# Optimization experiments

Hardware: AMD Instinct MI355X
Metric: run time of the kernel (lower is better)

## Reference

```python
import jax, jax.numpy as jnp
import numpy as np
from jax import lax

SPATIAL = 4
PAD = 1
STRIDE = 1


def _route(x, rconv_w, rconv_b, fc_w, fc_b, num_experts):
    # x: (b, c, h, w); adaptive avg pool to (SPATIAL, SPATIAL) -- h,w divisible by SPATIAL
    b, c, h, w = x.shape
    pooled = x.reshape(b, c, SPATIAL, h // SPATIAL, SPATIAL, w // SPATIAL).mean(axis=(3, 5))
    # 1x1 conv: (b,c,s,s) x (rc,c) -> (b,rc,s,s)
    y = jnp.einsum('bcij,rc->brij', pooled, rconv_w) + rconv_b[None, :, None, None]
    y = jax.nn.relu(y).reshape(b, -1)                      # (b, rc*s*s)
    y = jax.nn.relu(y @ fc_w.T + fc_b)                     # (b, num_experts*c)
    y = y.reshape(b, num_experts, c)
    return jax.nn.sigmoid(y)                               # (b, k, c)


def _conv_per_sample(xi, wi):
    # xi: (c_in, h, w), wi: (c_out, c_in, kh, kw)
    out = lax.conv_general_dilated(
        xi[None], wi, window_strides=(STRIDE, STRIDE),
        padding=[(PAD, PAD), (PAD, PAD)],
        dimension_numbers=('NCHW', 'OIHW', 'NCHW'))
    return out[0]


def setup_inputs() -> dict:
    key = jax.random.key(0)
    ks = jax.random.split(key, 6)
    b, c_in, c_out, kk, ne = 16, 256, 256, 3, 3
    rc = max(c_in // 16, 16)  # reduction_channels = 16
    x = jax.random.normal(ks[0], (b, c_in, 64, 64), dtype=jnp.float32)
    expert_weight = jax.random.normal(ks[1], (ne, c_out, c_in, kk, kk), dtype=jnp.float32) * 0.02
    rconv_w = jax.random.normal(ks[2], (rc, c_in), dtype=jnp.float32) * 0.05
    rconv_b = jax.random.normal(ks[3], (rc,), dtype=jnp.float32) * 0.05
    fc_w = jax.random.normal(ks[4], (ne * c_in, rc * SPATIAL * SPATIAL), dtype=jnp.float32) * 0.05
    fc_b = jax.random.normal(ks[5], (ne * c_in,), dtype=jnp.float32) * 0.05
    return {"x": x, "expert_weight": expert_weight, "rconv_w": rconv_w,
            "rconv_b": rconv_b, "fc_w": fc_w, "fc_b": fc_b}


def reference(x, expert_weight, rconv_w, rconv_b, fc_w, fc_b):
    ne = expert_weight.shape[0]
    r = _route(x, rconv_w, rconv_b, fc_w, fc_b, ne)        # (b, k, c_in)
    # per-sample combined weights: routing scales input channels of each expert kernel
    w = jnp.einsum('bkc,kocij->bocij', r, expert_weight)    # (b, c_out, c_in, kh, kw)
    out = jax.vmap(_conv_per_sample)(x, w)                  # (b, c_out, h', w')
    return out
```

## Files before the change

kernel.cpp:

```cpp
#include <hip/hip_runtime.h>

#define B_   16
#define C_   256
#define OC_  256
#define H_   64
#define W_   64

typedef __attribute__((ext_vector_type(8))) __bf16 bf16x8;
typedef __attribute__((ext_vector_type(4))) float  f32x4;

__device__ __forceinline__ short f2bf(float f) {
    unsigned u = __float_as_uint(f);
    u += 0x7fffu + ((u >> 16) & 1u);
    return (short)(u >> 16);
}
__device__ __forceinline__ unsigned pk2(float a, float b) {
    return (unsigned(f2bf(a)) & 0xffffu) | (unsigned(f2bf(b)) << 16);
}
__device__ __forceinline__ void gll16(const void* g, void* l) {
    __builtin_amdgcn_global_load_lds(
        (const __attribute__((address_space(1))) unsigned int*)g,
        (__attribute__((address_space(3))) unsigned int*)l,
        16, 0, 0);
}

__global__ __launch_bounds__(256) void k_transpose_pool(
        const float* __restrict__ x, short* __restrict__ xt, float* __restrict__ pooled) {
    int y = blockIdx.x, b = blockIdx.y, t = threadIdx.x;
    int si = y >> 4;
    int lane = t & 63, wv = t >> 6;
    int xq = lane & 15, cw = lane >> 4;
    __shared__ float tile[64 * 67];

    for (int cc = 0; cc < 4; ++cc) {
        int cbase = cc * 64;
        if (cc) __syncthreads();
        #pragma unroll
        for (int r = 0; r < 4; ++r) {
            int c_l = r * 16 + wv * 4 + cw;
            float4 v = *(const float4*)&x[(((size_t)b * C_ + cbase + c_l) * H_ + y) * W_ + xq * 4];
            float* tp = &tile[c_l * 67 + xq * 4];
            tp[0] = v.x; tp[1] = v.y; tp[2] = v.z; tp[3] = v.w;
            float s = v.x + v.y + v.z + v.w;
            s += __shfl_xor(s, 1);
            s += __shfl_xor(s, 2);
            if ((lane & 3) == 0)
                atomicAdd(&pooled[((b * 4 + si) * 4 + (xq >> 2)) * 256 + cbase + c_l], s);
        }
        __syncthreads();
        #pragma unroll
        for (int r2 = 0; r2 < 2; ++r2) {
            int u = r2 * 256 + t;
            int xx = u >> 3, cgl = u & 7;
            float f[8];
            #pragma unroll
            for (int j = 0; j < 8; ++j) f[j] = tile[(cgl * 8 + j) * 67 + xx];
            uint4 pkv;
            pkv.x = pk2(f[0], f[1]); pkv.y = pk2(f[2], f[3]);
            pkv.z = pk2(f[4], f[5]); pkv.w = pk2(f[6], f[7]);
            *(uint4*)&xt[(((size_t)b * H_ + y) * W_ + xx) * C_ + cbase + cgl * 8] = pkv;
        }
    }
}

__global__ __launch_bounds__(256) void k_route(
        const float* __restrict__ pooled, const float* __restrict__ rconv_w,
        const float* __restrict__ rconv_b, const float* __restrict__ fc_w,
        const float* __restrict__ fc_b, float* __restrict__ r_buf) {
    int b = blockIdx.x;
    int t = threadIdx.x;
    __shared__ float pl[16][257];
    __shared__ float y1[256];

    #pragma unroll
    for (int q = 0; q < 16; ++q)
        pl[q][t] = pooled[b * 4096 + q * 256 + t] * (1.0f / 256.0f);
    __syncthreads();
    {
        int rcc = t >> 4, ss = t & 15;
        float acc = rconv_b[rcc];
        #pragma unroll 8
        for (int c = 0; c < 256; ++c)
            acc += pl[ss][c] * rconv_w[rcc * 256 + c];
        y1[rcc * 16 + ss] = fmaxf(acc, 0.f);
    }
    __syncthreads();
    for (int e0 = 0; e0 < 768; e0 += 256) {
        int e = e0 + t;
        float acc = fc_b[e];
        #pragma unroll 8
        for (int q = 0; q < 256; ++q)
            acc += y1[q] * fc_w[(size_t)e * 256 + q];
        acc = fmaxf(acc, 0.f);
        r_buf[(size_t)b * 768 + e] = 1.f / (1.f + __expf(-acc));
    }
}

__global__ __launch_bounds__(256) void k_combine(
        const float* __restrict__ E, const float* __restrict__ r_buf,
        short* __restrict__ wcomb) {
    int o = blockIdx.x;
    int b0 = blockIdx.y * 4;
    int t = threadIdx.x;
    __shared__ float eT[3][2304];
    #pragma unroll
    for (int k = 0; k < 3; ++k)
        #pragma unroll
        for (int q = 0; q < 9; ++q)
            eT[k][q * 256 + t] = E[((size_t)k * OC_ + o) * 2304 + q * 256 + t];
    __syncthreads();
    int c = t;
    #pragma unroll
    for (int bb = 0; bb < 4; ++bb) {
        int b = b0 + bb;
        float r0 = r_buf[(size_t)b * 768 + c];
        float r1 = r_buf[(size_t)b * 768 + 256 + c];
        float r2 = r_buf[(size_t)b * 768 + 512 + c];
        short* wo = wcomb + ((size_t)(b * OC_ + o) * 9) * C_;
        #pragma unroll
        for (int tap = 0; tap < 9; ++tap) {
            float v = r0 * eT[0][c * 9 + tap] + r1 * eT[1][c * 9 + tap]
                    + r2 * eT[2][c * 9 + tap];
            wo[tap * C_ + c] = f2bf(v);
        }
    }
}

__global__ __launch_bounds__(256, 2) void k_conv(
        const short* __restrict__ xt, const short* __restrict__ wcomb,
        float* __restrict__ out, const short* __restrict__ zbuf) {
    int lin  = blockIdx.x;
    int work = (lin & 7) * 128 + (lin >> 3);
    int b      = work >> 6;
    int o_base = ((work >> 5) & 1) * 128;
    int y0     = (work & 31) * 2;

    int t = threadIdx.x;
    int lane = t & 63, w = t >> 6;
    int quad = lane >> 4, l15 = lane & 15;

    __shared__ __align__(16) short win[4 * 64 * 64];
    __shared__ __align__(16) short abuf[2][128 * 64];

    const short* wsrc[8];
    #pragma unroll
    for (int r = 0; r < 8; ++r) {
        int u = r * 256 + t;
        int pos = u >> 3, sp = u & 7;
        int wrow = pos >> 6, xc = pos & 63;
        int yy = y0 - 1 + wrow;
        int ss = sp ^ (xc & 7);
        wsrc[r] = ((unsigned)yy < 64u)
            ? xt + (((size_t)b * 64 + yy) * 64 + xc) * 256 + ss * 8
            : zbuf;
    }
    const short* asrc[4];
    #pragma unroll
    for (int r = 0; r < 4; ++r) {
        int u = r * 256 + t;
        int o_l = u >> 3, sp = u & 7;
        int ss = sp ^ (o_l & 7);
        asrc[r] = wcomb + (((size_t)b * 256 + o_base + o_l) * 9) * 256 + ss * 8;
    }

    int m_base = (w & 1) * 64;
    int n_base = (w >> 1) * 64;
    int ry0 = n_base >> 6;
    int xb[4];
    #pragma unroll
    for (int nb = 0; nb < 4; ++nb) xb[nb] = nb * 16 + l15;

    f32x4 acc[4][4];
    #pragma unroll
    for (int i = 0; i < 4; ++i)
        #pragma unroll
        for (int j = 0; j < 4; ++j) acc[i][j] = {0.f, 0.f, 0.f, 0.f};

    for (int cc = 0; cc < 4; ++cc) {
        int ccOff = cc * 64;
        #pragma unroll
        for (int r = 0; r < 8; ++r)
            gll16(wsrc[r] + ccOff, &win[(r * 256 + w * 64) * 8]);
        #pragma unroll
        for (int r = 0; r < 4; ++r)
            gll16(asrc[r] + ccOff, &abuf[0][(r * 256 + w * 64) * 8]);
        __syncthreads();

        #pragma unroll
        for (int tap = 0; tap < 9; ++tap) {
            const int ti = tap / 3, tj = tap % 3;
            const int cur = tap & 1;
            if (tap < 8) {
                int off2 = (tap + 1) * 256 + ccOff;
                #pragma unroll
                for (int r = 0; r < 4; ++r)
                    gll16(asrc[r] + off2, &abuf[cur ^ 1][(r * 256 + w * 64) * 8]);
            }
            int wrb = (ry0 + ti) * 4096;
            #pragma unroll
            for (int s = 0; s < 2; ++s) {
                int slog = s * 4 + quad;
                bf16x8 af[4], bv[4];
                #pragma unroll
                for (int mb = 0; mb < 4; ++mb) {
                    int o_l = m_base + mb * 16 + l15;
                    af[mb] = *(const bf16x8*)&abuf[cur][o_l * 64 + ((slog ^ (o_l & 7)) * 8)];
                }
                #pragma unroll
                for (int nb = 0; nb < 4; ++nb) {
                    int xc = xb[nb] + (tj - 1);
                    bool ok = ((unsigned)xc < 64u);
                    int xs = ok ? xc : 0;
                    bf16x8 v = *(const bf16x8*)&win[wrb + xs * 64 + ((slog ^ (xs & 7)) * 8)];
                    bf16x8 zz = {};
                    bv[nb] = ok ? v : zz;
                }
                #pragma unroll
                for (int mb = 0; mb < 4; ++mb)
                    #pragma unroll
                    for (int nb = 0; nb < 4; ++nb)
                        acc[mb][nb] = __builtin_amdgcn_mfma_f32_16x16x32_bf16(
                            af[mb], bv[nb], acc[mb][nb], 0, 0, 0);
            }
            __syncthreads();
        }
    }

    #pragma unroll
    for (int mb = 0; mb < 4; ++mb) {
        #pragma unroll
        for (int nb = 0; nb < 4; ++nb) {
            int p  = n_base + nb * 16 + l15;
            int yy = y0 + (p >> 6);
            int xx = p & 63;
            #pragma unroll
            for (int rg = 0; rg < 4; ++rg) {
                int o = o_base + m_base + mb * 16 + quad * 4 + rg;
                out[(((size_t)b * OC_ + o) * H_ + yy) * W_ + xx] = acc[mb][nb][rg];
            }
        }
    }
}

extern "C" void kernel_launch(void* const* d_in, const int* in_sizes, int n_in,
                              void* d_out, int out_size, void* d_ws, size_t ws_size,
                              hipStream_t stream) {
    const float* x       = (const float*)d_in[0];
    const float* E       = (const float*)d_in[1];
    const float* rconv_w = (const float*)d_in[2];
    const float* rconv_b = (const float*)d_in[3];
    const float* fc_w    = (const float*)d_in[4];
    const float* fc_b    = (const float*)d_in[5];
    float* out = (float*)d_out;

    char* ws = (char*)d_ws;
    short* xt     = (short*)(ws);
    short* wcomb  = (short*)(ws + 33554432);
    float* pooled = (float*)(ws + 52428800);
    short* zbuf   = (short*)(ws + 52690944);
    float* rbuf   = (float*)(ws + 52692992);

    hipMemsetAsync(pooled, 0, 262144 + 1024, stream);

    k_transpose_pool<<<dim3(64, 16), 256, 0, stream>>>(x, xt, pooled);
    k_route<<<dim3(16), 256, 0, stream>>>(pooled, rconv_w, rconv_b, fc_w, fc_b, rbuf);
    k_combine<<<dim3(256, 4), 256, 0, stream>>>(E, rbuf, wcomb);
    k_conv<<<dim3(1024), 256, 0, stream>>>(xt, wcomb, out, zbuf);
}
```

Baseline: 243.9 us.

## Replace pooling atomics with per-block partial sums reduced in route kernel

Measured after the change: 270.0 us. 1.11x slower.

```diff
diff --git a/kernel.cpp b/kernel.cpp
--- a/kernel.cpp
+++ b/kernel.cpp
@@ -25,46 +25,64 @@
 }
 
 __global__ __launch_bounds__(256) void k_transpose_pool(
-        const float* __restrict__ x, short* __restrict__ xt, float* __restrict__ pooled) {
-    int y = blockIdx.x, b = blockIdx.y, t = threadIdx.x;
-    int si = y >> 4;
+        const float* __restrict__ x, short* __restrict__ xt,
+        float* __restrict__ pp2) {
+    int g = blockIdx.x, b = blockIdx.y, t = threadIdx.x;
     int lane = t & 63, wv = t >> 6;
     int xq = lane & 15, cw = lane >> 4;
     __shared__ float tile[64 * 67];
 
-    for (int cc = 0; cc < 4; ++cc) {
-        int cbase = cc * 64;
-        if (cc) __syncthreads();
-        #pragma unroll
-        for (int r = 0; r < 4; ++r) {
-            int c_l = r * 16 + wv * 4 + cw;
-            float4 v = *(const float4*)&x[(((size_t)b * C_ + cbase + c_l) * H_ + y) * W_ + xq * 4];
-            float* tp = &tile[c_l * 67 + xq * 4];
-            tp[0] = v.x; tp[1] = v.y; tp[2] = v.z; tp[3] = v.w;
-            float s = v.x + v.y + v.z + v.w;
-            s += __shfl_xor(s, 1);
-            s += __shfl_xor(s, 2);
-            if ((lane & 3) == 0)
-                atomicAdd(&pooled[((b * 4 + si) * 4 + (xq >> 2)) * 256 + cbase + c_l], s);
-        }
-        __syncthreads();
-        #pragma unroll
-        for (int r2 = 0; r2 < 2; ++r2) {
-            int u = r2 * 256 + t;
-            int xx = u >> 3, cgl = u & 7;
-            float f[8];
-            #pragma unroll
-            for (int j = 0; j < 8; ++j) f[j] = tile[(cgl * 8 + j) * 67 + xx];
-            uint4 pkv;
-            pkv.x = pk2(f[0], f[1]); pkv.y = pk2(f[2], f[3]);
-            pkv.z = pk2(f[4], f[5]); pkv.w = pk2(f[6], f[7]);
-            *(uint4*)&xt[(((size_t)b * H_ + y) * W_ + xx) * C_ + cbase + cgl * 8] = pkv;
-        }
+    float racc[4][4];
+    #pragma unroll
+    for (int i = 0; i < 4; ++i)
+        #pragma unroll
+        for (int j = 0; j < 4; ++j) racc[i][j] = 0.f;
+
+    for (int iy = 0; iy < 4; ++iy) {
+        int y = g * 4 + iy;
+        for (int cc = 0; cc < 4; ++cc) {
+            int cbase = cc * 64;
+            if (iy | cc) __syncthreads();
+            #pragma unroll
+            for (int r = 0; r < 4; ++r) {
+                int c_l = r * 16 + wv * 4 + cw;
+                float4 v = *(const float4*)&x[(((size_t)b * C_ + cbase + c_l) * H_ + y) * W_ + xq * 4];
+                float* tp = &tile[c_l * 67 + xq * 4];
+                tp[0] = v.x; tp[1] = v.y; tp[2] = v.z; tp[3] = v.w;
+                float s = v.x + v.y + v.z + v.w;
+                s += __shfl_xor(s, 1);
+                s += __shfl_xor(s, 2);
+                racc[cc][r] += s;
+            }
+            __syncthreads();
+            #pragma unroll
+            for (int r2 = 0; r2 < 2; ++r2) {
+                int u = r2 * 256 + t;
+                int xx = u >> 3, cgl = u & 7;
+                float f[8];
+                #pragma unroll
+                for (int j = 0; j < 8; ++j) f[j] = tile[(cgl * 8 + j) * 67 + xx];
+                uint4 pkv;
+                pkv.x = pk2(f[0], f[1]); pkv.y = pk2(f[2], f[3]);
+                pkv.z = pk2(f[4], f[5]); pkv.w = pk2(f[6], f[7]);
+                *(uint4*)&xt[(((size_t)b * H_ + y) * W_ + xx) * C_ + cbase + cgl * 8] = pkv;
+            }
+        }
+    }
+    if ((lane & 3) == 0) {
+        int sj = xq >> 2;
+        #pragma unroll
+        for (int cc = 0; cc < 4; ++cc)
+            #pragma unroll
+            for (int r = 0; r < 4; ++r) {
+                int c = cc * 64 + r * 16 + wv * 4 + cw;
+                pp2[((b * 16 + g) * 4 + sj) * 256 + c] = racc[cc][r];
+            }
     }
 }
 
 __global__ __launch_bounds__(256) void k_route(
-        const float* __restrict__ pooled, const float* __restrict__ rconv_w,
+        const float* __restrict__ pp2, const float* __restrict__ rconv_w,
         const float* __restrict__ rconv_b, const float* __restrict__ fc_w,
         const float* __restrict__ fc_b, float* __restrict__ r_buf) {
     int b = blockIdx.x;
@@ -73,8 +91,14 @@
     __shared__ float y1[256];
 
     #pragma unroll
-    for (int q = 0; q < 16; ++q)
-        pl[q][t] = pooled[b * 4096 + q * 256 + t] * (1.0f / 256.0f);
+    for (int q = 0; q < 16; ++q) {
+        int si = q >> 2, sj = q & 3;
+        float s = 0.f;
+        #pragma unroll
+        for (int gg = 0; gg < 4; ++gg)
+            s += pp2[((b * 16 + si * 4 + gg) * 4 + sj) * 256 + t];
+        pl[q][t] = s * (1.0f / 256.0f);
+    }
     __syncthreads();
     {
         int rcc = t >> 4, ss = t & 15;
@@ -100,7 +124,7 @@
         const float* __restrict__ E, const float* __restrict__ r_buf,
         short* __restrict__ wcomb) {
     int o = blockIdx.x;
-    int b0 = blockIdx.y * 4;
+    int b0 = blockIdx.y * 8;
     int t = threadIdx.x;
     __shared__ float eT[3][2304];
     #pragma unroll
@@ -111,7 +135,7 @@
     __syncthreads();
     int c = t;
     #pragma unroll
-    for (int bb = 0; bb < 4; ++bb) {
+    for (int bb = 0; bb < 8; ++bb) {
         int b = b0 + bb;
         float r0 = r_buf[(size_t)b * 768 + c];
         float r1 = r_buf[(size_t)b * 768 + 256 + c];
@@ -254,16 +278,16 @@
     float* out = (float*)d_out;
 
     char* ws = (char*)d_ws;
-    short* xt     = (short*)(ws);
-    short* wcomb  = (short*)(ws + 33554432);
-    float* pooled = (float*)(ws + 52428800);
-    short* zbuf   = (short*)(ws + 52690944);
-    float* rbuf   = (float*)(ws + 52692992);
-
-    hipMemsetAsync(pooled, 0, 262144 + 1024, stream);
-
-    k_transpose_pool<<<dim3(64, 16), 256, 0, stream>>>(x, xt, pooled);
-    k_route<<<dim3(16), 256, 0, stream>>>(pooled, rconv_w, rconv_b, fc_w, fc_b, rbuf);
-    k_combine<<<dim3(256, 4), 256, 0, stream>>>(E, rbuf, wcomb);
+    short* xt    = (short*)(ws);
+    short* wcomb = (short*)(ws + 33554432);
+    float* pp2   = (float*)(ws + 52428800);
+    float* rbuf  = (float*)(ws + 53477376);
+    short* zbuf  = (short*)(ws + 53526528);
+
+    hipMemsetAsync(zbuf, 0, 1024, stream);
+
+    k_transpose_pool<<<dim3(16, 16), 256, 0, stream>>>(x, xt, pp2);
+    k_route<<<dim3(16), 256, 0, stream>>>(pp2, rconv_w, rconv_b, fc_w, fc_b, rbuf);
+    k_combine<<<dim3(256, 2), 256, 0, stream>>>(E, rbuf, wcomb);
     k_conv<<<dim3(1024), 256, 0, stream>>>(xt, wcomb, out, zbuf);
 }
```
